# Kernel optimization log

Hardware: AMD Instinct MI355X
Metric: run time of the kernel (lower is better)

Reference implementation:

```python
import jax, jax.numpy as jnp
import numpy as np

B, L, D = 4, 2048, 512
NL, ED, N, R, K = 2, 1024, 16, 32, 4
EPS = 1e-5


def rmsnorm(x, w):
    return x * jax.lax.rsqrt(jnp.mean(x * x, axis=-1, keepdims=True) + EPS) * w


def mamba_block(u, in_w, conv_w, conv_b, xproj_w, dtproj_w, dtproj_b, A_log, Dp, out_w):
    # u: [B, L, D]
    xz = u @ in_w.T                              # [B, L, 2*ED]
    xp, z = jnp.split(xz, 2, axis=-1)
    # depthwise causal conv1d over time
    xc = jnp.transpose(xp, (0, 2, 1))            # [B, ED, L]
    w = conv_w[:, None, :]                       # [ED, 1, K]
    xc = jax.lax.conv_general_dilated(
        xc, w, window_strides=(1,), padding=[(K - 1, 0)],
        feature_group_count=ED, dimension_numbers=('NCH', 'OIH', 'NCH'))
    xc = jnp.transpose(xc, (0, 2, 1)) + conv_b   # [B, L, ED]
    xc = jax.nn.silu(xc)
    # input-dependent SSM params
    dbc = xc @ xproj_w.T                         # [B, L, R+2N]
    dt, Bm, Cm = jnp.split(dbc, [R, R + N], axis=-1)
    delta = jax.nn.softplus(dt @ dtproj_w.T + dtproj_b)  # [B, L, ED]
    A = -jnp.exp(A_log)                          # [ED, N]
    # sequential selective scan over time (carry h: [B, ED, N])
    dT = jnp.transpose(delta, (1, 0, 2))
    BT = jnp.transpose(Bm, (1, 0, 2))
    CT = jnp.transpose(Cm, (1, 0, 2))
    xT = jnp.transpose(xc, (1, 0, 2))

    def step(h, inp):
        d_t, B_t, C_t, x_t = inp                 # [B,ED], [B,N], [B,N], [B,ED]
        dA = jnp.exp(d_t[..., None] * A)         # [B, ED, N]
        h = dA * h + (d_t * x_t)[..., None] * B_t[:, None, :]
        y = jnp.einsum('ben,bn->be', h, C_t)
        return h, y

    h0 = jnp.zeros((u.shape[0], ED, N), u.dtype)
    _, yT = jax.lax.scan(step, h0, (dT, BT, CT, xT))
    y = jnp.transpose(yT, (1, 0, 2)) + Dp * xc   # [B, L, ED]
    y = y * jax.nn.silu(z)
    return y @ out_w.T                           # [B, L, D]


def setup_inputs() -> dict:
    key = jax.random.key(0)
    ks = jax.random.split(key, 10)
    s = 0.02
    return {
        'x': jax.random.normal(ks[0], (B, L, D), jnp.float32),
        'mask': jnp.ones((B, L), jnp.int32),
        'norm_w': jnp.ones((NL, D), jnp.float32),
        'in_w': jax.random.normal(ks[1], (NL, 2 * ED, D), jnp.float32) * s,
        'conv_w': jax.random.normal(ks[2], (NL, ED, K), jnp.float32) * 0.2,
        'conv_b': jnp.zeros((NL, ED), jnp.float32),
        'xproj_w': jax.random.normal(ks[3], (NL, R + 2 * N, ED), jnp.float32) * s,
        'dtproj_w': jax.random.normal(ks[4], (NL, ED, R), jnp.float32) * s,
        'dtproj_b': jax.random.normal(ks[5], (NL, ED), jnp.float32) * 0.1,
        'A_log': jnp.broadcast_to(jnp.log(jnp.arange(1, N + 1, dtype=jnp.float32)), (NL, ED, N)) + 0.0,
        'D_param': jnp.ones((NL, ED), jnp.float32),
        'out_w': jax.random.normal(ks[6], (NL, D, ED), jnp.float32) * s,
    }


def reference(x, mask, norm_w, in_w, conv_w, conv_b, xproj_w, dtproj_w,
              dtproj_b, A_log, D_param, out_w):
    m = mask.astype(x.dtype)[:, :, None]
    for i in range(norm_w.shape[0]):
        x = x * m
        # ResidualBlock: x + MambaBlock(RMSNorm(x)); dropout is identity at eval
        x = x + mamba_block(rmsnorm(x, norm_w[i]), in_w[i], conv_w[i], conv_b[i],
                            xproj_w[i], dtproj_w[i], dtproj_b[i], A_log[i],
                            D_param[i], out_w[i])
        x = x * m
    return x, x[:, 0, :]
```

## Files before the change

### kernel.cpp

```cpp
#include <hip/hip_runtime.h>
#include <math.h>

#define B_ 4
#define L_ 2048
#define D_ 512
#define ED_ 1024
#define N_ 16
#define R_ 32
#define KC_ 4
#define M_ (B_*L_)
#define NC_ 64
#define T_  (L_/NC_)
#define S_  (B_*ED_*N_)
#define LOG2E 1.44269504f
#define LN2   0.69314718f

typedef __attribute__((ext_vector_type(8))) short short8;
typedef __attribute__((ext_vector_type(4))) float floatx4;
typedef __attribute__((ext_vector_type(2))) float floatv2;

static __device__ __forceinline__ float b2f(unsigned short u) {
    unsigned int v = ((unsigned int)u) << 16;
    float f;
    __builtin_memcpy(&f, &v, 4);
    return f;
}
static __device__ __forceinline__ unsigned short f2b(float f) {
    unsigned int u;
    __builtin_memcpy(&u, &f, 4);
    unsigned int lsb = (u >> 16) & 1u;
    u += 0x7fffu + lsb;
    return (unsigned short)(u >> 16);
}
static __device__ __forceinline__ float silu(float x) {
    return x / (1.f + exp2f(-LOG2E * x));
}
static __device__ __forceinline__ float softplusf(float x) {
    return fmaxf(x, 0.f) + LN2 * log2f(1.f + exp2f(-LOG2E * fabsf(x)));
}
static __device__ __forceinline__ void pow_tree2(float a1, floatv2* pw) {
    float a2 = a1 * a1, a4 = a2 * a2, a8 = a4 * a4;
    pw[0] = (floatv2){a1, a2};
    pw[1] = pw[0] * a2;
    pw[2] = pw[0] * a4;
    pw[3] = pw[1] * a4;
    pw[4] = pw[0] * a8;
    pw[5] = pw[1] * a8;
    pw[6] = pw[2] * a8;
    pw[7] = pw[3] * a8;
}

__global__ void k_flag0(int* flag) {
    if (blockIdx.x == 0 && threadIdx.x == 0) *flag = 0;
}
__global__ void k_detect(const unsigned short* __restrict__ x, int* flag) {
    int i = blockIdx.x * 256 + threadIdx.x;
    unsigned int e = (x[i] >> 7) & 0xFF;
    unsigned long long m = __ballot(e >= 0x88);
    if ((threadIdx.x & 63) == 0 && m != 0ull) atomicOr(flag, 1);
}

struct Seg9 { const void* src[9]; int prefix[10]; };
__global__ void k_cvt_batch(Seg9 segs, float* __restrict__ dst, int total,
                            const int* __restrict__ flag) {
    int i = blockIdx.x * 256 + threadIdx.x;
    if (i >= total) return;
    int s = 0;
#pragma unroll
    for (int k = 1; k < 9; ++k) if (i >= segs.prefix[k]) s = k;
    int off = i - segs.prefix[s];
    if (*flag) dst[i] = ((const float*)segs.src[s])[off];
    else       dst[i] = b2f(((const unsigned short*)segs.src[s])[off]);
}
__global__ void k_cvt_bf_batch(const void* __restrict__ src0,
                               const void* __restrict__ src1,
                               unsigned short* __restrict__ dst,
                               int n0, int total, const int* __restrict__ flag) {
    int i = blockIdx.x * 256 + threadIdx.x;
    if (i >= total) return;
    const void* src = (i < n0) ? src0 : src1;
    int off = (i < n0) ? i : i - n0;
    if (*flag) dst[i] = f2b(((const float*)src)[off]);
    else       dst[i] = ((const unsigned short*)src)[off];
}

__global__ __launch_bounds__(128) void k_rmsnorm(float* __restrict__ x,
                                                 const int* __restrict__ mask,
                                                 const float* __restrict__ w,
                                                 unsigned short* __restrict__ ubf) {
    int row = blockIdx.x;
    int tid = threadIdx.x;
    size_t base = (size_t)row * D_ + tid * 4;
    float4 v = *(const float4*)(x + base);
    float mv = (float)mask[row];
    v.x *= mv; v.y *= mv; v.z *= mv; v.w *= mv;
    *(float4*)(x + base) = v;
    float ss = v.x*v.x + v.y*v.y + v.z*v.z + v.w*v.w;
#pragma unroll
    for (int o = 1; o < 64; o <<= 1) ss += __shfl_xor(ss, o, 64);
    __shared__ float sred[2];
    if ((tid & 63) == 0) sred[tid >> 6] = ss;
    __syncthreads();
    float rs = rsqrtf((sred[0] + sred[1]) / (float)D_ + 1e-5f);
    float4 wv = *(const float4*)(w + tid * 4);
    ushort4 b4;
    b4.x = f2b(v.x * rs * wv.x);
    b4.y = f2b(v.y * rs * wv.y);
    b4.z = f2b(v.z * rs * wv.z);
    b4.w = f2b(v.w * rs * wv.w);
    *(ushort4*)(ubf + base) = b4;
}

typedef __attribute__((address_space(1))) const unsigned int guint;
typedef __attribute__((address_space(3))) unsigned int luint;
#define GLL(gp, lp) __builtin_amdgcn_global_load_lds((guint*)(const void*)(gp), (luint*)(void*)(lp), 16, 0, 0)

template<int N> static __device__ __forceinline__ void waitv() {
    if constexpr (N == 0) asm volatile("s_waitcnt vmcnt(0)" ::: "memory");
    else if constexpr (N == 3) asm volatile("s_waitcnt vmcnt(3)" ::: "memory");
    else if constexpr (N == 4) asm volatile("s_waitcnt vmcnt(4)" ::: "memory");
}

template<int MODE, int BNT>
__global__ __launch_bounds__(256) void gemm_bt(const unsigned short* __restrict__ A,
                                               const unsigned short* __restrict__ W,
                                               void* __restrict__ C,
                                               const int* __restrict__ mask,
                                               const int* __restrict__ flag,
                                               void* __restrict__ out,
                                               int M, int N, int K) {
    constexpr int NF = BNT / 32;
    constexpr int LW = 2 + BNT / 64;
    __shared__ unsigned short As[3][128][32];
    __shared__ unsigned short Bs[3][BNT][32];
    int tid  = threadIdx.x;
    int wave = tid >> 6;
    int lane = tid & 63;
    int nwg = gridDim.x * gridDim.y;
    int id  = blockIdx.y * gridDim.x + blockIdx.x;
    int swz = (id & 7) * (nwg >> 3) + (id >> 3);
    int m0 = (swz / gridDim.x) * 128;
    int n0 = (swz % gridDim.x) * BNT;
    int wm = (wave & 1) * 64;
    int wn = (wave >> 1) * (BNT / 2);
    int quad = lane >> 4;
    int l16  = lane & 15;
    int crd = (quad ^ ((l16 >> 1) & 3)) * 8;

    int rA0 = wave * 16 + (lane >> 2);
    int cA  = ((lane & 3) ^ ((rA0 >> 1) & 3)) * 8;

    floatx4 acc[4][NF] = {};

    auto stage = [&](int buf, int k0) {
        const unsigned short* gA0 = A + (size_t)(m0 + rA0) * K + k0 + cA;
        GLL(gA0,                   &As[buf][wave * 16][0]);
        GLL(gA0 + (size_t)64 * K,  &As[buf][64 + wave * 16][0]);
        const unsigned short* gB0 = W + (size_t)(n0 + rA0) * K + k0 + cA;
        GLL(gB0,                   &Bs[buf][wave * 16][0]);
        if constexpr (BNT == 128)
            GLL(gB0 + (size_t)64 * K, &Bs[buf][64 + wave * 16][0]);
    };

    int nk = K / 32;
    stage(0, 0);
    stage(1, 32);

    int cur = 0;
    for (int t = 0; t < nk; ++t) {
        if (t + 1 < nk) waitv<LW>();
        else            waitv<0>();
        asm volatile("s_barrier" ::: "memory");
        if (t + 2 < nk) {
            int bw = cur + 2; if (bw >= 3) bw -= 3;
            stage(bw, (t + 2) * 32);
        }
        short8 af[4], bfr[NF];
#pragma unroll
        for (int f = 0; f < 4; ++f)
            af[f]  = *(const short8*)&As[cur][wm + f * 16 + l16][crd];
#pragma unroll
        for (int f = 0; f < NF; ++f)
            bfr[f] = *(const short8*)&Bs[cur][wn + f * 16 + l16][crd];
#pragma unroll
        for (int mf = 0; mf < 4; ++mf)
#pragma unroll
            for (int nf = 0; nf < NF; ++nf)
                acc[mf][nf] = __builtin_amdgcn_mfma_f32_16x16x32_bf16(af[mf], bfr[nf], acc[mf][nf], 0, 0, 0);
        asm volatile("s_waitcnt lgkmcnt(0)" ::: "memory");
        cur = (cur == 2) ? 0 : cur + 1;
    }

    int fl = (MODE == 3) ? *flag : 0;
#pragma unroll
    for (int mf = 0; mf < 4; ++mf) {
#pragma unroll
        for (int nf = 0; nf < NF; ++nf) {
#pragma unroll
            for (int i = 0; i < 4; ++i) {
                int r = m0 + wm + mf * 16 + quad * 4 + i;
                int c = n0 + wn + nf * 16 + l16;
                size_t idx = (size_t)r * N + c;
                if (MODE == 1) {
                    ((unsigned short*)C)[idx] = f2b(acc[mf][nf][i]);
                } else if (MODE == 2) {
                    float* C32 = (float*)C;
                    float mv = (float)mask[r];
                    C32[idx] = (C32[idx] + acc[mf][nf][i]) * mv;
                } else {
                    const float* C32 = (const float*)C;
                    float mv = (float)mask[r];
                    float v = (C32[idx] + acc[mf][nf][i]) * mv;
                    if (fl) ((float*)out)[idx] = v;
                    else    ((unsigned short*)out)[idx] = f2b(v);
                    if ((r & (L_ - 1)) == 0) {
                        size_t oidx = (size_t)M_ * D_ + (size_t)(r >> 11) * D_ + c;
                        if (fl) ((float*)out)[oidx] = v;
                        else    ((unsigned short*)out)[oidx] = f2b(v);
                    }
                }
            }
        }
    }
}

#define BM 64
#define BN 64
#define BK 16
#define KS 8
__global__ __launch_bounds__(256) void gemm_nt_sk(const float* __restrict__ A,
                                                  const float* __restrict__ W,
                                                  float* __restrict__ part,
                                                  int M, int N, int K) {
    __shared__ float Asm[BK][BM + 4];
    __shared__ float Wsm[BK][BN + 4];
    int tid = threadIdx.x;
    int ks = blockIdx.x;
    int m0 = blockIdx.y * BM;
    int kb = ks * (K / KS);
    int ke = kb + (K / KS);
    int tx = tid & 15;
    int ty = tid >> 4;
    int lr = tid >> 2;
    int lk = (tid & 3) * 4;
    float acc[4][4] = {};
    for (int k0 = kb; k0 < ke; k0 += BK) {
        float4 av = *(const float4*)(A + (size_t)(m0 + lr) * K + k0 + lk);
        Asm[lk + 0][lr] = av.x; Asm[lk + 1][lr] = av.y;
        Asm[lk + 2][lr] = av.z; Asm[lk + 3][lr] = av.w;
        float4 wv = *(const float4*)(W + (size_t)lr * K + k0 + lk);
        Wsm[lk + 0][lr] = wv.x; Wsm[lk + 1][lr] = wv.y;
        Wsm[lk + 2][lr] = wv.z; Wsm[lk + 3][lr] = wv.w;
        __syncthreads();
#pragma unroll
        for (int kk = 0; kk < BK; ++kk) {
            float4 a = *(const float4*)&Asm[kk][ty * 4];
            float4 w = *(const float4*)&Wsm[kk][tx * 4];
            acc[0][0] += a.x * w.x; acc[0][1] += a.x * w.y; acc[0][2] += a.x * w.z; acc[0][3] += a.x * w.w;
            acc[1][0] += a.y * w.x; acc[1][1] += a.y * w.y; acc[1][2] += a.y * w.z; acc[1][3] += a.y * w.w;
            acc[2][0] += a.z * w.x; acc[2][1] += a.z * w.y; acc[2][2] += a.z * w.z; acc[2][3] += a.z * w.w;
            acc[3][0] += a.w * w.x; acc[3][1] += a.w * w.y; acc[3][2] += a.w * w.z; acc[3][3] += a.w * w.w;
        }
        __syncthreads();
    }
    float* p = part + (size_t)ks * M * N;
#pragma unroll
    for (int i = 0; i < 4; ++i) {
        int m = m0 + ty * 4 + i;
#pragma unroll
        for (int j = 0; j < 4; ++j) {
            int n = tx * 4 + j;
            p[(size_t)m * N + n] = acc[i][j];
        }
    }
}

__global__ void k_red8(const float* __restrict__ part, float* __restrict__ dbc, int mn4) {
    int i = blockIdx.x * 256 + threadIdx.x;
    if (i >= mn4) return;
    float4 s = ((const float4*)part)[i];
#pragma unroll
    for (int ks = 1; ks < KS; ++ks) {
        float4 v = ((const float4*)(part + (size_t)ks * mn4 * 4))[i];
        s.x += v.x; s.y += v.y; s.z += v.z; s.w += v.w;
    }
    ((float4*)dbc)[i] = s;
}

__global__ __launch_bounds__(256) void k_conv(const unsigned short* __restrict__ xzb,
                                              const float* __restrict__ cw,
                                              const float* __restrict__ cb,
                                              float* __restrict__ xc) {
    int idx = blockIdx.x * 256 + threadIdx.x;
    int e2 = idx & (ED_ / 2 - 1);
    int e  = e2 * 2;
    int bl = idx >> 9;
    int l  = bl & (L_ - 1);
    float acc0 = cb[e], acc1 = cb[e + 1];
    const unsigned short* col = xzb + (size_t)bl * (2 * ED_) + e;
    float4 wa = *(const float4*)(cw + e * 4);
    float4 wb = *(const float4*)(cw + e * 4 + 4);
    ushort2 v3 = *(const ushort2*)(col);
    if (l >= 3) {
        ushort2 v0 = *(const ushort2*)(col - 3 * 2 * ED_);
        ushort2 v1 = *(const ushort2*)(col - 2 * 2 * ED_);
        ushort2 v2 = *(const ushort2*)(col - 1 * 2 * ED_);
        acc0 += wa.x * b2f(v0.x) + wa.y * b2f(v1.x) + wa.z * b2f(v2.x) + wa.w * b2f(v3.x);
        acc1 += wb.x * b2f(v0.y) + wb.y * b2f(v1.y) + wb.z * b2f(v2.y) + wb.w * b2f(v3.y);
    } else {
        if (l >= 2) {
            ushort2 v1 = *(const ushort2*)(col - 2 * 2 * ED_);
            acc0 += wa.y * b2f(v1.x); acc1 += wb.y * b2f(v1.y);
        }
        if (l >= 1) {
            ushort2 v2 = *(const ushort2*)(col - 1 * 2 * ED_);
            acc0 += wa.z * b2f(v2.x); acc1 += wb.z * b2f(v2.y);
        }
        acc0 += wa.w * b2f(v3.x); acc1 += wb.w * b2f(v3.y);
    }
    float2 o; o.x = silu(acc0); o.y = silu(acc1);
    *(float2*)(xc + (size_t)bl * ED_ + e) = o;
}

__global__ __launch_bounds__(256) void k_scan_a(const float* __restrict__ xc,
                                                const float* __restrict__ dbc,
                                                const float* __restrict__ A_log,
                                                const float* __restrict__ dtw,
                                                const float* __restrict__ dtb,
                                                float* __restrict__ delta,
                                                float* __restrict__ pa,
                                                float* __restrict__ hl) {
    int b = blockIdx.z, c = blockIdx.y;
    int e = blockIdx.x * 256 + threadIdx.x;
    __shared__ float sRow[T_][64];
    size_t t0 = (size_t)b * L_ + (size_t)c * T_;
    {
        const float4* src = (const float4*)(dbc + t0 * 64);
        float4* dst = (float4*)&sRow[0][0];
        dst[threadIdx.x]       = src[threadIdx.x];
        dst[threadIdx.x + 256] = src[threadIdx.x + 256];
    }
    __syncthreads();
    floatv2 w2[R_ / 2];
    const floatv2* wp2 = (const floatv2*)(dtw + (size_t)e * R_);
#pragma unroll
    for (int i = 0; i < R_ / 2; ++i) w2[i] = wp2[i];
    float bias = dtb[e];
    float A0 = -exp2f(LOG2E * A_log[e * N_]) * LOG2E;
    bool structured = true;
#pragma unroll
    for (int n = 1; n < N_; ++n) {
        float An = -exp2f(LOG2E * A_log[e * N_ + n]) * LOG2E;
        structured = structured && (fabsf(An - (n + 1) * A0) <= 1e-4f * fabsf(An));
    }
    floatv2 h2[8];
#pragma unroll
    for (int i = 0; i < 8; ++i) h2[i] = (floatv2){0.f, 0.f};
    float sumd = 0.f;
    if (structured) {
        const float* xp = xc + t0 * ED_ + e;
        float* dep = delta + t0 * ED_ + e;
        float xv_t = *xp; xp += ED_;
        for (int t = 0; t < T_; ++t) {
            float xv_n = (t + 1 < T_) ? *xp : 0.f; xp += ED_;
            const floatv2* dt2 = (const floatv2*)&sRow[t][0];
            floatv2 q0 = {0.f, 0.f}, q1 = {0.f, 0.f}, q2 = {0.f, 0.f}, q3 = {0.f, 0.f};
#pragma unroll
            for (int r = 0; r < R_ / 2; r += 4) {
                q0 += dt2[r + 0] * w2[r + 0];
                q1 += dt2[r + 1] * w2[r + 1];
                q2 += dt2[r + 2] * w2[r + 2];
                q3 += dt2[r + 3] * w2[r + 3];
            }
            floatv2 qs = (q0 + q1) + (q2 + q3);
            float d = softplusf(qs.x + qs.y + bias);
            *dep = d; dep += ED_;
            float dx = d * xv_t;
            sumd += d;
            floatv2 pw[8];
            pow_tree2(exp2f(d * A0), pw);
            const floatv2* bb2 = (const floatv2*)&sRow[t][32];
#pragma unroll
            for (int i = 0; i < 8; ++i)
                h2[i] = pw[i] * h2[i] + dx * bb2[i];
            xv_t = xv_n;
        }
    } else {
        float A[N_];
        float* h = (float*)h2;
#pragma unroll
        for (int n = 0; n < N_; ++n) A[n] = -exp2f(LOG2E * A_log[e * N_ + n]) * LOG2E;
        float* wsc = (float*)w2;
        for (int t = 0; t < T_; ++t) {
            size_t bl = t0 + t;
            float p0 = bias, p1 = 0.f, p2 = 0.f, p3 = 0.f;
#pragma unroll
            for (int r = 0; r < R_; r += 4) {
                p0 += sRow[t][r + 0] * wsc[r + 0];
                p1 += sRow[t][r + 1] * wsc[r + 1];
                p2 += sRow[t][r + 2] * wsc[r + 2];
                p3 += sRow[t][r + 3] * wsc[r + 3];
            }
            float d = softplusf((p0 + p1) + (p2 + p3));
            delta[bl * ED_ + e] = d;
            float dx = d * xc[bl * ED_ + e];
            sumd += d;
#pragma unroll
            for (int n = 0; n < N_; ++n) {
                float a = exp2f(d * A[n]);
                h[n] = a * h[n] + dx * sRow[t][32 + n];
            }
        }
    }
    size_t s = (size_t)c * S_ + ((size_t)b * ED_ + e) * N_;
    const float* h = (const float*)h2;
#pragma unroll
    for (int n = 0; n < N_; ++n) {
        float An = -exp2f(LOG2E * A_log[e * N_ + n]) * LOG2E;
        pa[s + n] = exp2f(sumd * An);
        hl[s + n] = h[n];
    }
}

__global__ __launch_bounds__(256) void k_scan_b(const float* __restrict__ pa,
                                                const float* __restrict__ hl,
                                                float* __restrict__ carry) {
    int s = blockIdx.x * 256 + threadIdx.x;
    float par[8], hlr[8];
#pragma unroll
    for (int c = 0; c < 8; ++c) {
        par[c] = pa[(size_t)c * S_ + s];
        hlr[c] = hl[(size_t)c * S_ + s];
    }
    float h = 0.f;
#pragma unroll
    for (int c = 0; c < NC_; ++c) {
        int r = c & 7;
        carry[(size_t)c * S_ + s] = h;
        float p = par[r], q = hlr[r];
        if (c + 8 < NC_) {
            par[r] = pa[(size_t)(c + 8) * S_ + s];
            hlr[r] = hl[(size_t)(c + 8) * S_ + s];
        }
        h = p * h + q;
    }
}

__global__ __launch_bounds__(256) void k_scan_c(const float* __restrict__ delta,
                                                const float* __restrict__ xc,
                                                const float* __restrict__ dbc,
                                                const unsigned short* __restrict__ xzb,
                                                const float* __restrict__ A_log,
                                                const float* __restrict__ Dp,
                                                const float* __restrict__ carry,
                                                unsigned short* __restrict__ ybf) {
    int b = blockIdx.z, c = blockIdx.y;
    int e = blockIdx.x * 256 + threadIdx.x;
    __shared__ float sRow[T_][64];
    size_t t0 = (size_t)b * L_ + (size_t)c * T_;
    {
        const float4* src = (const float4*)(dbc + t0 * 64);
        float4* dst = (float4*)&sRow[0][0];
        dst[threadIdx.x]       = src[threadIdx.x];
        dst[threadIdx.x + 256] = src[threadIdx.x + 256];
    }
    __syncthreads();
    float A0 = -exp2f(LOG2E * A_log[e * N_]) * LOG2E;
    bool structured = true;
#pragma unroll
    for (int n = 1; n < N_; ++n) {
        float An = -exp2f(LOG2E * A_log[e * N_ + n]) * LOG2E;
        structured = structured && (fabsf(An - (n + 1) * A0) <= 1e-4f * fabsf(An));
    }
    floatv2 h2[8];
    size_t s = (size_t)c * S_ + ((size_t)b * ED_ + e) * N_;
    {
        const floatv2* cp = (const floatv2*)(carry + s);
#pragma unroll
        for (int i = 0; i < 8; ++i) h2[i] = cp[i];
    }
    float Dv = Dp[e];
    if (structured) {
        const float* dp_ = delta + t0 * ED_ + e;
        const float* xp  = xc    + t0 * ED_ + e;
        const unsigned short* zp = xzb + t0 * (2 * ED_) + ED_ + e;
        unsigned short* yp = ybf + t0 * ED_ + e;
        float d_t  = *dp_; dp_ += ED_;
        float xv_t = *xp;  xp  += ED_;
        unsigned short z_t = *zp; zp += 2 * ED_;
        for (int t = 0; t < T_; ++t) {
            float d_n = 0.f, xv_n = 0.f;
            unsigned short z_n = 0;
            if (t + 1 < T_) {
                d_n  = *dp_;
                xv_n = *xp;
                z_n  = *zp;
            }
            dp_ += ED_; xp += ED_; zp += 2 * ED_;
            float dx = d_t * xv_t;
            floatv2 pw[8];
            pow_tree2(exp2f(d_t * A0), pw);
            const floatv2* bb2 = (const floatv2*)&sRow[t][32];
            const floatv2* cc2 = (const floatv2*)&sRow[t][48];
            floatv2 y0 = {0.f, 0.f}, y1 = {0.f, 0.f};
#pragma unroll
            for (int i = 0; i < 8; i += 2) {
                h2[i + 0] = pw[i + 0] * h2[i + 0] + dx * bb2[i + 0];
                h2[i + 1] = pw[i + 1] * h2[i + 1] + dx * bb2[i + 1];
                y0 += h2[i + 0] * cc2[i + 0];
                y1 += h2[i + 1] * cc2[i + 1];
            }
            floatv2 ys = y0 + y1;
            float y = ys.x + ys.y;
            float z = b2f(z_t);
            *yp = f2b((y + Dv * xv_t) * silu(z)); yp += ED_;
            d_t = d_n; xv_t = xv_n; z_t = z_n;
        }
    } else {
        float A[N_];
        float* h = (float*)h2;
#pragma unroll
        for (int n = 0; n < N_; ++n) A[n] = -exp2f(LOG2E * A_log[e * N_ + n]) * LOG2E;
        for (int t = 0; t < T_; ++t) {
            size_t bl = t0 + t;
            float d  = delta[bl * ED_ + e];
            float xv = xc[bl * ED_ + e];
            float dx = d * xv;
            float y = 0.f;
#pragma unroll
            for (int n = 0; n < N_; ++n) {
                float a = exp2f(d * A[n]);
                h[n] = a * h[n] + dx * sRow[t][32 + n];
                y += h[n] * sRow[t][48 + n];
            }
            float z = b2f(xzb[bl * (2 * ED_) + ED_ + e]);
            ybf[bl * ED_ + e] = f2b((y + Dv * xv) * silu(z));
        }
    }
}

extern "C" void kernel_launch(void* const* d_in, const int* in_sizes, int n_in,
                              void* d_out, int out_size, void* d_ws, size_t ws_size,
                              hipStream_t stream) {
    const int* mask = (const int*)d_in[1];

    float* ws = (float*)d_ws;
    int*   flag = (int*)d_ws;
    float* xw   = ws + 16;
    float* wn   = xw   + (size_t)M_ * D_;
    float* wc   = wn   + 1024;
    float* wcb  = wc   + 8192;
    float* wx   = wcb  + 2048;
    float* wdt  = wx   + 131072;
    float* wdtb = wdt  + 65536;
    float* wal  = wdtb + 2048;
    float* wdp  = wal  + 32768;
    unsigned short* wib = (unsigned short*)(wdp + 2048);
    unsigned short* wob = wib + 2097152;
    unsigned short* ubf = wob + 1048576;
    unsigned short* xzb = ubf + (size_t)M_ * D_;
    float* xc   = (float*)(xzb + (size_t)M_ * 2 * ED_);
    float* dbc  = xc    + (size_t)M_ * ED_;
    float* delta= dbc   + (size_t)M_ * 64;
    float* carry= delta + (size_t)M_ * ED_;
    float* pa   = carry + (size_t)NC_ * S_;
    float* hl   = pa    + (size_t)NC_ * S_;
    unsigned short* ybf = (unsigned short*)pa;
    float* part = carry;

    k_flag0<<<1, 1, 0, stream>>>(flag);
    k_detect<<<128, 256, 0, stream>>>((const unsigned short*)d_in[0], flag);

    {
        Seg9 segs;
        int idxs[9] = {0, 2, 4, 5, 6, 7, 8, 9, 10};
        int pre = 0;
        for (int i = 0; i < 9; ++i) {
            segs.src[i] = d_in[idxs[i]];
            segs.prefix[i] = pre;
            pre += in_sizes[idxs[i]];
        }
        segs.prefix[9] = pre;
        k_cvt_batch<<<(pre + 255) / 256, 256, 0, stream>>>(segs, xw, pre, flag);
        int n0 = 2 * 2 * ED_ * D_;
        int tot = n0 + 2 * D_ * ED_;
        k_cvt_bf_batch<<<(tot + 255) / 256, 256, 0, stream>>>(d_in[3], d_in[11], wib, n0, tot, flag);
    }

    for (int layer = 0; layer < 2; ++layer) {
        const float* nw = wn  + layer * D_;
        const unsigned short* iw = wib + (size_t)layer * 2 * ED_ * D_;
        const float* cw = wc  + layer * ED_ * KC_;
        const float* cb = wcb + layer * ED_;
        const float* xwp= wx  + (size_t)layer * 64 * ED_;
        const float* dw = wdt + (size_t)layer * ED_ * R_;
        const float* db = wdtb+ layer * ED_;
        const float* al = wal + layer * ED_ * N_;
        const float* dp = wdp + layer * ED_;
        const unsigned short* ow = wob + (size_t)layer * D_ * ED_;

        k_rmsnorm<<<M_, 128, 0, stream>>>(xw, mask, nw, ubf);
        gemm_bt<1, 128><<<dim3(2 * ED_ / 128, M_ / 128), 256, 0, stream>>>(ubf, iw, xzb, nullptr, nullptr, nullptr, M_, 2 * ED_, D_);
        k_conv<<<(M_ * ED_ / 2) / 256, 256, 0, stream>>>(xzb, cw, cb, xc);
        gemm_nt_sk<<<dim3(KS, M_ / BM), 256, 0, stream>>>(xc, xwp, part, M_, 64, ED_);
        k_red8<<<(M_ * 64 / 4 + 255) / 256, 256, 0, stream>>>(part, dbc, M_ * 64 / 4);
        k_scan_a<<<dim3(ED_ / 256, NC_, B_), 256, 0, stream>>>(xc, dbc, al, dw, db, delta, pa, hl);
        k_scan_b<<<S_ / 256, 256, 0, stream>>>(pa, hl, carry);
        k_scan_c<<<dim3(ED_ / 256, NC_, B_), 256, 0, stream>>>(delta, xc, dbc, xzb, al, dp, carry, ybf);
        if (layer == 0) {
            gemm_bt<2, 64><<<dim3(D_ / 64, M_ / 128), 256, 0, stream>>>(ybf, ow, xw, mask, nullptr, nullptr, M_, D_, ED_);
        } else {
            gemm_bt<3, 64><<<dim3(D_ / 64, M_ / 128), 256, 0, stream>>>(ybf, ow, xw, mask, flag, d_out, M_, D_, ED_);
        }
    }
}
```

Baseline: 528.8 us.

## Recompute delta in scan pass C, store chunk sums instead of decay products

The delta tensor is no longer written by scan pass A and read back in pass C. Pass C recomputes the dt projection and softplus from shared-memory rows. Pass A now stores one scalar sum of delta per (chunk, batch, channel) instead of sixteen decay products, and the carry kernel rebuilds those products with exp2. The chunk count is doubled to 128, which gives more parallel blocks but makes the serial carry pass longer and its buffers larger. Overall the change trades memory traffic for extra arithmetic in pass C.

```diff
diff --git a/kernel.cpp b/kernel.cpp
--- a/kernel.cpp
+++ b/kernel.cpp
@@ -9,7 +9,7 @@
 #define R_ 32
 #define KC_ 4
 #define M_ (B_*L_)
-#define NC_ 64
+#define NC_ 128
 #define T_  (L_/NC_)
 #define S_  (B_*ED_*N_)
 #define LOG2E 1.44269504f
@@ -327,8 +327,7 @@
                                                 const float* __restrict__ A_log,
                                                 const float* __restrict__ dtw,
                                                 const float* __restrict__ dtb,
-                                                float* __restrict__ delta,
-                                                float* __restrict__ pa,
+                                                float* __restrict__ sumdbuf,
                                                 float* __restrict__ hl) {
     int b = blockIdx.z, c = blockIdx.y;
     int e = blockIdx.x * 256 + threadIdx.x;
@@ -336,9 +335,7 @@
     size_t t0 = (size_t)b * L_ + (size_t)c * T_;
     {
         const float4* src = (const float4*)(dbc + t0 * 64);
-        float4* dst = (float4*)&sRow[0][0];
-        dst[threadIdx.x]       = src[threadIdx.x];
-        dst[threadIdx.x + 256] = src[threadIdx.x + 256];
+        ((float4*)&sRow[0][0])[threadIdx.x] = src[threadIdx.x];
     }
     __syncthreads();
     floatv2 w2[R_ / 2];
@@ -359,7 +356,6 @@
     float sumd = 0.f;
     if (structured) {
         const float* xp = xc + t0 * ED_ + e;
-        float* dep = delta + t0 * ED_ + e;
         float xv_t = *xp; xp += ED_;
         for (int t = 0; t < T_; ++t) {
             float xv_n = (t + 1 < T_) ? *xp : 0.f; xp += ED_;
@@ -374,7 +370,6 @@
             }
             floatv2 qs = (q0 + q1) + (q2 + q3);
             float d = softplusf(qs.x + qs.y + bias);
-            *dep = d; dep += ED_;
             float dx = d * xv_t;
             sumd += d;
             floatv2 pw[8];
@@ -402,7 +397,6 @@
                 p3 += sRow[t][r + 3] * wsc[r + 3];
             }
             float d = softplusf((p0 + p1) + (p2 + p3));
-            delta[bl * ED_ + e] = d;
             float dx = d * xc[bl * ED_ + e];
             sumd += d;
 #pragma unroll
@@ -415,21 +409,21 @@
     size_t s = (size_t)c * S_ + ((size_t)b * ED_ + e) * N_;
     const float* h = (const float*)h2;
 #pragma unroll
-    for (int n = 0; n < N_; ++n) {
-        float An = -exp2f(LOG2E * A_log[e * N_ + n]) * LOG2E;
-        pa[s + n] = exp2f(sumd * An);
-        hl[s + n] = h[n];
-    }
-}
-
-__global__ __launch_bounds__(256) void k_scan_b(const float* __restrict__ pa,
+    for (int n = 0; n < N_; ++n) hl[s + n] = h[n];
+    sumdbuf[(size_t)c * (B_ * ED_) + (size_t)b * ED_ + e] = sumd;
+}
+
+__global__ __launch_bounds__(256) void k_scan_b(const float* __restrict__ sumd,
                                                 const float* __restrict__ hl,
+                                                const float* __restrict__ A_log,
                                                 float* __restrict__ carry) {
     int s = blockIdx.x * 256 + threadIdx.x;
-    float par[8], hlr[8];
+    float An = -exp2f(LOG2E * A_log[s & (ED_ * N_ - 1)]) * LOG2E;
+    int be = s >> 4;
+    float sdr[8], hlr[8];
 #pragma unroll
     for (int c = 0; c < 8; ++c) {
-        par[c] = pa[(size_t)c * S_ + s];
+        sdr[c] = sumd[(size_t)c * (B_ * ED_) + be];
         hlr[c] = hl[(size_t)c * S_ + s];
     }
     float h = 0.f;
@@ -437,20 +431,21 @@
     for (int c = 0; c < NC_; ++c) {
         int r = c & 7;
         carry[(size_t)c * S_ + s] = h;
-        float p = par[r], q = hlr[r];
+        float p = exp2f(sdr[r] * An), q = hlr[r];
         if (c + 8 < NC_) {
-            par[r] = pa[(size_t)(c + 8) * S_ + s];
+            sdr[r] = sumd[(size_t)(c + 8) * (B_ * ED_) + be];
             hlr[r] = hl[(size_t)(c + 8) * S_ + s];
         }
         h = p * h + q;
     }
 }
 
-__global__ __launch_bounds__(256) void k_scan_c(const float* __restrict__ delta,
-                                                const float* __restrict__ xc,
+__global__ __launch_bounds__(256) void k_scan_c(const float* __restrict__ xc,
                                                 const float* __restrict__ dbc,
                                                 const unsigned short* __restrict__ xzb,
                                                 const float* __restrict__ A_log,
+                                                const float* __restrict__ dtw,
+                                                const float* __restrict__ dtb,
                                                 const float* __restrict__ Dp,
                                                 const float* __restrict__ carry,
                                                 unsigned short* __restrict__ ybf) {
@@ -460,11 +455,14 @@
     size_t t0 = (size_t)b * L_ + (size_t)c * T_;
     {
         const float4* src = (const float4*)(dbc + t0 * 64);
-        float4* dst = (float4*)&sRow[0][0];
-        dst[threadIdx.x]       = src[threadIdx.x];
-        dst[threadIdx.x + 256] = src[threadIdx.x + 256];
+        ((float4*)&sRow[0][0])[threadIdx.x] = src[threadIdx.x];
     }
     __syncthreads();
+    floatv2 w2[R_ / 2];
+    const floatv2* wp2 = (const floatv2*)(dtw + (size_t)e * R_);
+#pragma unroll
+    for (int i = 0; i < R_ / 2; ++i) w2[i] = wp2[i];
+    float bias = dtb[e];
     float A0 = -exp2f(LOG2E * A_log[e * N_]) * LOG2E;
     bool structured = true;
 #pragma unroll
@@ -481,22 +479,30 @@
     }
     float Dv = Dp[e];
     if (structured) {
-        const float* dp_ = delta + t0 * ED_ + e;
-        const float* xp  = xc    + t0 * ED_ + e;
+        const float* xp  = xc  + t0 * ED_ + e;
         const unsigned short* zp = xzb + t0 * (2 * ED_) + ED_ + e;
         unsigned short* yp = ybf + t0 * ED_ + e;
-        float d_t  = *dp_; dp_ += ED_;
         float xv_t = *xp;  xp  += ED_;
         unsigned short z_t = *zp; zp += 2 * ED_;
         for (int t = 0; t < T_; ++t) {
-            float d_n = 0.f, xv_n = 0.f;
+            float xv_n = 0.f;
             unsigned short z_n = 0;
             if (t + 1 < T_) {
-                d_n  = *dp_;
                 xv_n = *xp;
                 z_n  = *zp;
             }
-            dp_ += ED_; xp += ED_; zp += 2 * ED_;
+            xp += ED_; zp += 2 * ED_;
+            const floatv2* dt2 = (const floatv2*)&sRow[t][0];
+            floatv2 q0 = {0.f, 0.f}, q1 = {0.f, 0.f}, q2 = {0.f, 0.f}, q3 = {0.f, 0.f};
+#pragma unroll
+            for (int r = 0; r < R_ / 2; r += 4) {
+                q0 += dt2[r + 0] * w2[r + 0];
+                q1 += dt2[r + 1] * w2[r + 1];
+                q2 += dt2[r + 2] * w2[r + 2];
+                q3 += dt2[r + 3] * w2[r + 3];
+            }
+            floatv2 qs = (q0 + q1) + (q2 + q3);
+            float d_t = softplusf(qs.x + qs.y + bias);
             float dx = d_t * xv_t;
             floatv2 pw[8];
             pow_tree2(exp2f(d_t * A0), pw);
@@ -514,16 +520,25 @@
             float y = ys.x + ys.y;
             float z = b2f(z_t);
             *yp = f2b((y + Dv * xv_t) * silu(z)); yp += ED_;
-            d_t = d_n; xv_t = xv_n; z_t = z_n;
+            xv_t = xv_n; z_t = z_n;
         }
     } else {
         float A[N_];
         float* h = (float*)h2;
 #pragma unroll
         for (int n = 0; n < N_; ++n) A[n] = -exp2f(LOG2E * A_log[e * N_ + n]) * LOG2E;
+        float* wsc = (float*)w2;
         for (int t = 0; t < T_; ++t) {
             size_t bl = t0 + t;
-            float d  = delta[bl * ED_ + e];
+            float p0 = bias, p1 = 0.f, p2 = 0.f, p3 = 0.f;
+#pragma unroll
+            for (int r = 0; r < R_; r += 4) {
+                p0 += sRow[t][r + 0] * wsc[r + 0];
+                p1 += sRow[t][r + 1] * wsc[r + 1];
+                p2 += sRow[t][r + 2] * wsc[r + 2];
+                p3 += sRow[t][r + 3] * wsc[r + 3];
+            }
+            float d = softplusf((p0 + p1) + (p2 + p3));
             float xv = xc[bl * ED_ + e];
             float dx = d * xv;
             float y = 0.f;
@@ -561,11 +576,10 @@
     unsigned short* xzb = ubf + (size_t)M_ * D_;
     float* xc   = (float*)(xzb + (size_t)M_ * 2 * ED_);
     float* dbc  = xc    + (size_t)M_ * ED_;
-    float* delta= dbc   + (size_t)M_ * 64;
-    float* carry= delta + (size_t)M_ * ED_;
-    float* pa   = carry + (size_t)NC_ * S_;
-    float* hl   = pa    + (size_t)NC_ * S_;
-    unsigned short* ybf = (unsigned short*)pa;
+    float* hl   = dbc   + (size_t)M_ * 64;
+    float* carry= hl    + (size_t)NC_ * S_;
+    float* sumd = carry + (size_t)NC_ * S_;
+    unsigned short* ybf = (unsigned short*)hl;
     float* part = carry;
 
     k_flag0<<<1, 1, 0, stream>>>(flag);
@@ -604,9 +618,9 @@
         k_conv<<<(M_ * ED_ / 2) / 256, 256, 0, stream>>>(xzb, cw, cb, xc);
         gemm_nt_sk<<<dim3(KS, M_ / BM), 256, 0, stream>>>(xc, xwp, part, M_, 64, ED_);
         k_red8<<<(M_ * 64 / 4 + 255) / 256, 256, 0, stream>>>(part, dbc, M_ * 64 / 4);
-        k_scan_a<<<dim3(ED_ / 256, NC_, B_), 256, 0, stream>>>(xc, dbc, al, dw, db, delta, pa, hl);
-        k_scan_b<<<S_ / 256, 256, 0, stream>>>(pa, hl, carry);
-        k_scan_c<<<dim3(ED_ / 256, NC_, B_), 256, 0, stream>>>(delta, xc, dbc, xzb, al, dp, carry, ybf);
+        k_scan_a<<<dim3(ED_ / 256, NC_, B_), 256, 0, stream>>>(xc, dbc, al, dw, db, sumd, hl);
+        k_scan_b<<<S_ / 256, 256, 0, stream>>>(sumd, hl, al, carry);
+        k_scan_c<<<dim3(ED_ / 256, NC_, B_), 256, 0, stream>>>(xc, dbc, xzb, al, dw, db, dp, carry, ybf);
         if (layer == 0) {
             gemm_bt<2, 64><<<dim3(D_ / 64, M_ / 128), 256, 0, stream>>>(ybf, ow, xw, mask, nullptr, nullptr, M_, D_, ED_);
         } else {
```

After: 509.6 us. 1.04x faster.
